# Kernel tuning notes

Measured on AMD Instinct MI355X. Metric: run time of the kernel, lower is better.

## Reference

```python
import jax, jax.numpy as jnp
import numpy as np

HIDDEN = 1024
NUM_HEADS = 16
HEAD_DIM = HIDDEN // NUM_HEADS


def setup_inputs() -> dict:
    key = jax.random.key(0)
    ks = jax.random.split(key, 11)
    s = 1.0 / np.sqrt(HIDDEN)
    x = jax.random.normal(ks[0], (4, 2048, HIDDEN), dtype=jnp.float32)
    Wq = jax.random.uniform(ks[1], (HIDDEN, HIDDEN), jnp.float32, -s, s)
    bq = jax.random.uniform(ks[2], (HIDDEN,), jnp.float32, -s, s)
    Wk = jax.random.uniform(ks[3], (HIDDEN, HIDDEN), jnp.float32, -s, s)
    bk = jax.random.uniform(ks[4], (HIDDEN,), jnp.float32, -s, s)
    Wv = jax.random.uniform(ks[5], (HIDDEN, HIDDEN), jnp.float32, -s, s)
    bv = jax.random.uniform(ks[6], (HIDDEN,), jnp.float32, -s, s)
    Wo = jax.random.uniform(ks[7], (HIDDEN, HIDDEN), jnp.float32, -s, s)
    bo = jax.random.uniform(ks[8], (HIDDEN,), jnp.float32, -s, s)
    ln_g = jnp.ones((HIDDEN,), jnp.float32)
    ln_b = jnp.zeros((HIDDEN,), jnp.float32)
    return {"x": x, "Wq": Wq, "bq": bq, "Wk": Wk, "bk": bk,
            "Wv": Wv, "bv": bv, "Wo": Wo, "bo": bo,
            "ln_g": ln_g, "ln_b": ln_b}


def _layer_norm(x, g, b, eps=1e-5):
    mu = jnp.mean(x, axis=-1, keepdims=True)
    var = jnp.var(x, axis=-1, keepdims=True)
    return (x - mu) * jax.lax.rsqrt(var + eps) * g + b


def reference(x, Wq, bq, Wk, bk, Wv, bv, Wo, bo, ln_g, ln_b):
    B, S, _ = x.shape
    residual = x
    h = _layer_norm(x, ln_g, ln_b)
    # projections (torch Linear: y = h @ W.T + b)
    q = (h @ Wq.T + bq).reshape(B, S, NUM_HEADS, HEAD_DIM).transpose(0, 2, 1, 3)
    k = (h @ Wk.T + bk).reshape(B, S, NUM_HEADS, HEAD_DIM).transpose(0, 2, 1, 3)
    v = (h @ Wv.T + bv).reshape(B, S, NUM_HEADS, HEAD_DIM).transpose(0, 2, 1, 3)
    scores = jnp.einsum('bhqd,bhkd->bhqk', q, k) / np.sqrt(HEAD_DIM).astype(np.float32)
    weights = jax.nn.softmax(scores, axis=-1)  # dropout = identity (eval mode)
    context = jnp.einsum('bhqk,bhkd->bhqd', weights, v)
    context = context.transpose(0, 2, 1, 3).reshape(B, S, HIDDEN)
    out = context @ Wo.T + bo
    return out + residual
```

## Files before the change

### kernel.cpp

```cpp
#include <hip/hip_runtime.h>

typedef unsigned short u16;
typedef unsigned int   u32;
using bf16x8 = __attribute__((ext_vector_type(8))) __bf16;
using f32x4  = __attribute__((ext_vector_type(4))) float;
using u32x2  = __attribute__((ext_vector_type(2))) unsigned int;

__device__ __forceinline__ u16 f2b(float f){
  union { float f; u32 i; } v; v.f = f;
  u32 r = v.i + 0x7FFFu + ((v.i >> 16) & 1u);
  return (u16)(r >> 16);
}
__device__ __forceinline__ u32 pk_bf16_trunc(float a, float b){
  return __builtin_amdgcn_perm(__float_as_uint(b), __float_as_uint(a), 0x07060302u);
}

__global__ __launch_bounds__(256) void cvt_w(const float* __restrict__ s0, const float* __restrict__ s1,
                                             const float* __restrict__ s2, const float* __restrict__ s3,
                                             u16* __restrict__ d){
  const float* srcs[4] = {s0, s1, s2, s3};
  const float* s = srcs[blockIdx.y];
  u16* dd = d + (size_t)blockIdx.y * (1024u * 1024u);
  const int i = (blockIdx.x * 256 + threadIdx.x) * 4;
  float4 v = *(const float4*)(s + i);
  uint2 o;
  o.x = (u32)f2b(v.x) | ((u32)f2b(v.y) << 16);
  o.y = (u32)f2b(v.z) | ((u32)f2b(v.w) << 16);
  *(uint2*)(dd + i) = o;
}

__global__ __launch_bounds__(256) void ln_kernel(const float* __restrict__ x, const float* __restrict__ g,
                                                 const float* __restrict__ be, u16* __restrict__ h){
  const int row = blockIdx.x, tid = threadIdx.x;
  const float* xr = x + (size_t)row * 1024u;
  float4 raw = *(const float4*)(xr + tid * 4);
  float s  = raw.x + raw.y + raw.z + raw.w;
  float sq = raw.x*raw.x + raw.y*raw.y + raw.z*raw.z + raw.w*raw.w;
  #pragma unroll
  for (int m = 1; m < 64; m <<= 1){ s += __shfl_xor(s, m); sq += __shfl_xor(sq, m); }
  __shared__ float ws[4], wq[4];
  if ((tid & 63) == 0){ ws[tid >> 6] = s; wq[tid >> 6] = sq; }
  __syncthreads();
  s  = ws[0] + ws[1] + ws[2] + ws[3];
  sq = wq[0] + wq[1] + wq[2] + wq[3];
  const float mu = s * (1.0f / 1024.0f);
  const float rstd = rsqrtf(sq * (1.0f / 1024.0f) - mu * mu + 1e-5f);
  float4 gg = *(const float4*)(g + tid * 4);
  float4 bb = *(const float4*)(be + tid * 4);
  float y0 = (raw.x - mu) * rstd * gg.x + bb.x;
  float y1 = (raw.y - mu) * rstd * gg.y + bb.y;
  float y2 = (raw.z - mu) * rstd * gg.z + bb.z;
  float y3 = (raw.w - mu) * rstd * gg.w + bb.w;
  uint2 outv;
  outv.x = (u32)f2b(y0) | ((u32)f2b(y1) << 16);
  outv.y = (u32)f2b(y2) | ((u32)f2b(y3) << 16);
  *(uint2*)(h + (size_t)row * 1024u + tid * 4) = outv;
}

__global__ __launch_bounds__(256) void gemm_qkv(const u16* __restrict__ A, const u16* __restrict__ Wcat,
                                                const float* __restrict__ bq, const float* __restrict__ bk,
                                                const float* __restrict__ bv,
                                                u16* __restrict__ qo, u16* __restrict__ ko, u16* __restrict__ vt){
  __shared__ u16 lds[8192];
  u16* lA = lds;
  u16* lB = lds + 4096;
  const int tid = threadIdx.x;
  const int lane = tid & 63, wv = tid >> 6, l15 = lane & 15, quad = lane >> 4;
  const int wr = wv >> 1, wc = wv & 1;
  const int row0 = blockIdx.x * 128, col0 = blockIdx.y * 128;
  const int K = 1024;

  const int r0_ = tid >> 2,         c0_ = tid & 3;
  const int r1_ = (256 + tid) >> 2, c1_ = (256 + tid) & 3;
  const u16* Asrc0 = A    + (size_t)(row0 + r0_) * K + (c0_ ^ ((r0_ >> 1) & 3)) * 8;
  const u16* Asrc1 = A    + (size_t)(row0 + r1_) * K + (c1_ ^ ((r1_ >> 1) & 3)) * 8;
  const u16* Bsrc0 = Wcat + (size_t)(col0 + r0_) * K + (c0_ ^ ((r0_ >> 1) & 3)) * 8;
  const u16* Bsrc1 = Wcat + (size_t)(col0 + r1_) * K + (c1_ ^ ((r1_ >> 1) & 3)) * 8;
  const int cr = (quad ^ ((l15 >> 1) & 3)) * 8;

  f32x4 acc[4][4] = {};
  for (int kt = 0; kt < 32; ++kt){
    __syncthreads();
    __builtin_amdgcn_global_load_lds(
      (const __attribute__((address_space(1))) void*)(Asrc0 + kt * 32),
      (__attribute__((address_space(3))) void*)(&lA[tid * 8]), 16, 0, 0);
    __builtin_amdgcn_global_load_lds(
      (const __attribute__((address_space(1))) void*)(Asrc1 + kt * 32),
      (__attribute__((address_space(3))) void*)(&lA[(256 + tid) * 8]), 16, 0, 0);
    __builtin_amdgcn_global_load_lds(
      (const __attribute__((address_space(1))) void*)(Bsrc0 + kt * 32),
      (__attribute__((address_space(3))) void*)(&lB[tid * 8]), 16, 0, 0);
    __builtin_amdgcn_global_load_lds(
      (const __attribute__((address_space(1))) void*)(Bsrc1 + kt * 32),
      (__attribute__((address_space(3))) void*)(&lB[(256 + tid) * 8]), 16, 0, 0);
    __syncthreads();
    bf16x8 af[4], bf[4];
    #pragma unroll
    for (int i = 0; i < 4; ++i) af[i] = *(const bf16x8*)&lA[(wr * 64 + i * 16 + l15) * 32 + cr];
    #pragma unroll
    for (int j = 0; j < 4; ++j) bf[j] = *(const bf16x8*)&lB[(wc * 64 + j * 16 + l15) * 32 + cr];
    #pragma unroll
    for (int i = 0; i < 4; ++i)
      #pragma unroll
      for (int j = 0; j < 4; ++j)
        acc[i][j] = __builtin_amdgcn_mfma_f32_16x16x32_bf16(af[i], bf[j], acc[i][j], 0, 0, 0);
  }
  const int sel = col0 >> 10;
  if (sel < 2){
    const float* bias = (sel == 0) ? bq : bk;
    u16* dst = (sel == 0) ? qo : ko;
    #pragma unroll
    for (int i = 0; i < 4; ++i){
      const int grow = row0 + wr * 64 + i * 16 + quad * 4;
      #pragma unroll
      for (int j = 0; j < 4; ++j){
        const int gcol = (col0 & 1023) + wc * 64 + j * 16 + l15;
        const float bb = bias[gcol];
        #pragma unroll
        for (int r = 0; r < 4; ++r){
          size_t off = (size_t)(grow + r) * 1024u + gcol;
          dst[off] = f2b(acc[i][j][r] + bb);
        }
      }
    }
  } else {
    __syncthreads();
    u16* pw = lds + wv * 2048;
    const int bglob = row0 >> 11;
    const int head  = ((col0 & 1023) >> 6) + wc;
    const int srem0 = (row0 & 2047) + wr * 64;
    const size_t vbase = (size_t)((bglob * 16 + head) * 64) * 2048u;
    #pragma unroll
    for (int p = 0; p < 2; ++p){
      #pragma unroll
      for (int i2 = 0; i2 < 2; ++i2){
        const int i = p * 2 + i2;
        #pragma unroll
        for (int j = 0; j < 4; ++j){
          const int d = j * 16 + l15;
          const float bv_ = bv[(col0 & 1023) + wc * 64 + d];
          const int u = (i2 * 4 + quad) ^ (d & 7);
          uint2 pk;
          pk.x = (u32)f2b(acc[i][j][0] + bv_) | ((u32)f2b(acc[i][j][1] + bv_) << 16);
          pk.y = (u32)f2b(acc[i][j][2] + bv_) | ((u32)f2b(acc[i][j][3] + bv_) << 16);
          *(uint2*)&pw[d * 32 + u * 4] = pk;
        }
      }
      const int dl = lane;
      #pragma unroll
      for (int c = 0; c < 4; ++c){
        const int u0 = (2 * c) ^ (dl & 7), u1 = (2 * c + 1) ^ (dl & 7);
        uint2 lo = *(const uint2*)&pw[dl * 32 + u0 * 4];
        uint2 hi = *(const uint2*)&pw[dl * 32 + u1 * 4];
        uint4 o4; o4.x = lo.x; o4.y = lo.y; o4.z = hi.x; o4.w = hi.y;
        *(uint4*)(vt + vbase + (size_t)dl * 2048u + srem0 + p * 32 + c * 8) = o4;
      }
    }
  }
}

__global__ __launch_bounds__(256) void gemm_out(const u16* __restrict__ A, const u16* __restrict__ W,
                                                const float* __restrict__ bias, const float* __restrict__ res,
                                                float* __restrict__ C, int M, int N, int K){
  __shared__ u16 lA[128 * 32];
  __shared__ u16 lB[128 * 32];
  const int tid = threadIdx.x;
  const int lane = tid & 63, wv = tid >> 6, l15 = lane & 15, quad = lane >> 4;
  const int wr = wv >> 1, wc = wv & 1;
  const int row0 = blockIdx.x * 128, col0 = blockIdx.y * 128;

  const int r0_ = tid >> 2,         c0_ = tid & 3;
  const int r1_ = (256 + tid) >> 2, c1_ = (256 + tid) & 3;
  const u16* Asrc0 = A + (size_t)(row0 + r0_) * K + (c0_ ^ ((r0_ >> 1) & 3)) * 8;
  const u16* Asrc1 = A + (size_t)(row0 + r1_) * K + (c1_ ^ ((r1_ >> 1) & 3)) * 8;
  const u16* Bsrc0 = W + (size_t)(col0 + r0_) * K + (c0_ ^ ((r0_ >> 1) & 3)) * 8;
  const u16* Bsrc1 = W + (size_t)(col0 + r1_) * K + (c1_ ^ ((r1_ >> 1) & 3)) * 8;
  const int cr = (quad ^ ((l15 >> 1) & 3)) * 8;

  f32x4 acc[4][4] = {};
  const int nkt = K >> 5;
  for (int kt = 0; kt < nkt; ++kt){
    __syncthreads();
    __builtin_amdgcn_global_load_lds(
      (const __attribute__((address_space(1))) void*)(Asrc0 + kt * 32),
      (__attribute__((address_space(3))) void*)(&lA[tid * 8]), 16, 0, 0);
    __builtin_amdgcn_global_load_lds(
      (const __attribute__((address_space(1))) void*)(Asrc1 + kt * 32),
      (__attribute__((address_space(3))) void*)(&lA[(256 + tid) * 8]), 16, 0, 0);
    __builtin_amdgcn_global_load_lds(
      (const __attribute__((address_space(1))) void*)(Bsrc0 + kt * 32),
      (__attribute__((address_space(3))) void*)(&lB[tid * 8]), 16, 0, 0);
    __builtin_amdgcn_global_load_lds(
      (const __attribute__((address_space(1))) void*)(Bsrc1 + kt * 32),
      (__attribute__((address_space(3))) void*)(&lB[(256 + tid) * 8]), 16, 0, 0);
    __syncthreads();
    bf16x8 af[4], bf[4];
    #pragma unroll
    for (int i = 0; i < 4; ++i) af[i] = *(const bf16x8*)&lA[(wr * 64 + i * 16 + l15) * 32 + cr];
    #pragma unroll
    for (int j = 0; j < 4; ++j) bf[j] = *(const bf16x8*)&lB[(wc * 64 + j * 16 + l15) * 32 + cr];
    #pragma unroll
    for (int i = 0; i < 4; ++i)
      #pragma unroll
      for (int j = 0; j < 4; ++j)
        acc[i][j] = __builtin_amdgcn_mfma_f32_16x16x32_bf16(af[i], bf[j], acc[i][j], 0, 0, 0);
  }
  #pragma unroll
  for (int i = 0; i < 4; ++i){
    const int grow = row0 + wr * 64 + i * 16 + quad * 4;
    #pragma unroll
    for (int j = 0; j < 4; ++j){
      const int gcol = col0 + wc * 64 + j * 16 + l15;
      const float bb = bias[gcol];
      #pragma unroll
      for (int r = 0; r < 4; ++r){
        size_t off = (size_t)(grow + r) * N + gcol;
        C[off] = acc[i][j][r] + bb + res[off];
      }
    }
  }
}

__global__ __launch_bounds__(256, 2) void attn_kernel(const u16* __restrict__ Q, const u16* __restrict__ K,
                                                      const u16* __restrict__ Vt, u16* __restrict__ O){
  __shared__ u16 kls[2][64 * 64];
  __shared__ u16 vls[2][64 * 64];
  const int tid = threadIdx.x;
  const int lane = tid & 63, wv = tid >> 6, l15 = lane & 15, quad = lane >> 4;
  const int bh = blockIdx.x & 63, qt = blockIdx.x >> 6;
  const int b = bh >> 4, hh = bh & 15;
  const int q0 = qt * 256;
  const u16* Qg = Q + ((size_t)b * 2048u) * 1024u + hh * 64;
  const u16* Kg = K + ((size_t)b * 2048u) * 1024u + hh * 64;
  const u16* Vg = Vt + (size_t)bh * 64u * 2048u;
  u16* Og = O + ((size_t)b * 2048u) * 1024u + hh * 64;

  const int sr = tid >> 3, sc = tid & 7, sr2 = sr + 32;
  const int sx = (sc ^ (sr & 7)) * 8;
  const int c0 = ((quad ^ (l15 & 7))) * 8;

  const float QSCALE = 0.125f * 1.44269504f;
  bf16x8 qf2[4][2];
  #pragma unroll
  for (int g = 0; g < 4; ++g)
    #pragma unroll
    for (int kk = 0; kk < 2; ++kk){
      qf2[g][kk] = *(const bf16x8*)(Qg + (size_t)(q0 + wv * 64 + g * 16 + l15) * 1024u + kk * 32 + quad * 8);
      #pragma unroll
      for (int e = 0; e < 8; ++e) qf2[g][kk][e] = (__bf16)((float)qf2[g][kk][e] * QSCALE);
    }

  bf16x8 ones_f;
  {
    const __bf16 onev = (__bf16)1.0f, zerov = (__bf16)0.0f;
    #pragma unroll
    for (int e = 0; e < 8; ++e) ones_f[e] = (l15 == 0) ? onev : zerov;
  }

  f32x4 o2[4][4] = {};
  f32x4 o_l[4] = {};
  const f32x4 zf = {0.f, 0.f, 0.f, 0.f};

  uint4 kr0, kr1, vr0, vr1;
  kr0 = *(const uint4*)(Kg + (size_t)sr  * 1024u + sc * 8);
  vr0 = *(const uint4*)(Vg + (size_t)sr  * 2048u + sc * 8);
  kr1 = *(const uint4*)(Kg + (size_t)sr2 * 1024u + sc * 8);
  vr1 = *(const uint4*)(Vg + (size_t)sr2 * 2048u + sc * 8);
  *(uint4*)&kls[0][sr  * 64 + sx] = kr0;
  *(uint4*)&vls[0][sr  * 64 + sx] = vr0;
  *(uint4*)&kls[0][sr2 * 64 + sx] = kr1;
  *(uint4*)&vls[0][sr2 * 64 + sx] = vr1;
  kr0 = *(const uint4*)(Kg + (size_t)(64 + sr)  * 1024u + sc * 8);
  vr0 = *(const uint4*)(Vg + (size_t)sr  * 2048u + 64 + sc * 8);
  kr1 = *(const uint4*)(Kg + (size_t)(64 + sr2) * 1024u + sc * 8);
  vr1 = *(const uint4*)(Vg + (size_t)sr2 * 2048u + 64 + sc * 8);
  __syncthreads();

  for (int kt = 0; kt < 32; ++kt){
    const int cur = kt & 1;
    const u16* kb = kls[cur];
    const u16* vb = vls[cur];
    if (kt < 31){
      u16* kw = kls[cur ^ 1];
      u16* vw = vls[cur ^ 1];
      *(uint4*)&kw[sr  * 64 + sx] = kr0;
      *(uint4*)&vw[sr  * 64 + sx] = vr0;
      *(uint4*)&kw[sr2 * 64 + sx] = kr1;
      *(uint4*)&vw[sr2 * 64 + sx] = vr1;
    }
    if (kt < 30){
      const int s0 = (kt + 2) * 64;
      kr0 = *(const uint4*)(Kg + (size_t)(s0 + sr)  * 1024u + sc * 8);
      vr0 = *(const uint4*)(Vg + (size_t)sr  * 2048u + s0 + sc * 8);
      kr1 = *(const uint4*)(Kg + (size_t)(s0 + sr2) * 1024u + sc * 8);
      vr1 = *(const uint4*)(Vg + (size_t)sr2 * 2048u + s0 + sc * 8);
    }

    f32x4 s2[4][4];
    #pragma unroll
    for (int j = 0; j < 4; ++j){
      const int rb = (j * 16 + l15) * 64;
      bf16x8 kfr0 = *(const bf16x8*)&kb[rb + c0];
      bf16x8 kfr1 = *(const bf16x8*)&kb[rb + (c0 ^ 32)];
      #pragma unroll
      for (int g = 0; g < 4; ++g){
        f32x4 a = __builtin_amdgcn_mfma_f32_16x16x32_bf16(kfr0, qf2[g][0], zf, 0, 0, 0);
        s2[g][j] = __builtin_amdgcn_mfma_f32_16x16x32_bf16(kfr1, qf2[g][1], a, 0, 0, 0);
      }
    }

    #pragma unroll
    for (int g = 0; g < 4; ++g)
      #pragma unroll
      for (int j = 0; j < 4; ++j)
        #pragma unroll
        for (int r = 0; r < 4; ++r)
          s2[g][j][r] = __builtin_amdgcn_exp2f(s2[g][j][r]);

    #pragma unroll
    for (int kk = 0; kk < 2; ++kk){
      bf16x8 afr[4];
      #pragma unroll
      for (int g = 0; g < 4; ++g){
        const int j0 = kk * 2, j1 = j0 + 1;
        u32 A0 = pk_bf16_trunc(s2[g][j0][0], s2[g][j0][1]);
        u32 A1 = pk_bf16_trunc(s2[g][j0][2], s2[g][j0][3]);
        u32 B0 = pk_bf16_trunc(s2[g][j1][0], s2[g][j1][1]);
        u32 B1 = pk_bf16_trunc(s2[g][j1][2], s2[g][j1][3]);
        u32x2 r1 = __builtin_amdgcn_permlane32_swap(A0, B0, false, false);
        u32x2 r2 = __builtin_amdgcn_permlane16_swap(r1[0], r1[1], false, false);
        u32x2 r3 = __builtin_amdgcn_permlane32_swap(A1, B1, false, false);
        u32x2 r4 = __builtin_amdgcn_permlane16_swap(r3[0], r3[1], false, false);
        union { uint4 u; bf16x8 v; } cv;
        cv.u.x = r2[0]; cv.u.y = r4[0]; cv.u.z = r2[1]; cv.u.w = r4[1];
        afr[g] = cv.v;
      }
      #pragma unroll
      for (int g = 0; g < 4; ++g)
        o_l[g] = __builtin_amdgcn_mfma_f32_16x16x32_bf16(afr[g], ones_f, o_l[g], 0, 0, 0);
      #pragma unroll
      for (int j2 = 0; j2 < 4; ++j2){
        bf16x8 bfr = *(const bf16x8*)&vb[(j2 * 16 + l15) * 64 + (c0 ^ (kk * 32))];
        #pragma unroll
        for (int g = 0; g < 4; ++g)
          o2[g][j2] = __builtin_amdgcn_mfma_f32_16x16x32_bf16(afr[g], bfr, o2[g][j2], 0, 0, 0);
      }
    }
    __syncthreads();
  }

  #pragma unroll
  for (int g = 0; g < 4; ++g){
    float lr[4];
    #pragma unroll
    for (int r = 0; r < 4; ++r) lr[r] = 1.0f / __shfl(o_l[g][r], quad * 16);
    #pragma unroll
    for (int j2 = 0; j2 < 4; ++j2){
      #pragma unroll
      for (int r = 0; r < 4; ++r){
        const int qrow = q0 + wv * 64 + g * 16 + quad * 4 + r;
        const int d = j2 * 16 + l15;
        Og[(size_t)qrow * 1024u + d] = f2b(o2[g][j2][r] * lr[r]);
      }
    }
  }
}

extern "C" void kernel_launch(void* const* d_in, const int* in_sizes, int n_in,
                              void* d_out, int out_size, void* d_ws, size_t ws_size,
                              hipStream_t stream){
  (void)in_sizes; (void)n_in; (void)out_size; (void)ws_size;
  const float* x   = (const float*)d_in[0];
  const float* Wq  = (const float*)d_in[1];
  const float* bq  = (const float*)d_in[2];
  const float* Wk  = (const float*)d_in[3];
  const float* bk  = (const float*)d_in[4];
  const float* Wv  = (const float*)d_in[5];
  const float* bv  = (const float*)d_in[6];
  const float* Wo  = (const float*)d_in[7];
  const float* bo  = (const float*)d_in[8];
  const float* lng = (const float*)d_in[9];
  const float* lnb = (const float*)d_in[10];
  float* out = (float*)d_out;

  const size_t TE = (size_t)8192 * 1024;
  u16* ws0 = (u16*)d_ws;
  u16* ws1 = ws0 + TE;
  u16* ws2 = ws1 + TE;
  u16* wsw = ws2 + TE;
  u16* wob = wsw + (size_t)3 * 1024 * 1024;
  u16* vt  = (u16*)d_out;

  cvt_w<<<dim3(1024, 4), 256, 0, stream>>>(Wq, Wk, Wv, Wo, wsw);
  ln_kernel<<<dim3(8192), 256, 0, stream>>>(x, lng, lnb, ws0);
  gemm_qkv<<<dim3(64, 24), 256, 0, stream>>>(ws0, wsw, bq, bk, bv, ws1, ws2, vt);
  attn_kernel<<<dim3(512), 256, 0, stream>>>(ws1, ws2, vt, ws1);
  gemm_out<<<dim3(64, 8), 256, 0, stream>>>(ws1, wob, bo, x, out, 8192, 1024, 1024);
}
```

Before: 275.4 us.

## Double-buffer LDS with register prefetch in QKV and output GEMMs

```diff
diff --git a/kernel.cpp b/kernel.cpp
--- a/kernel.cpp
+++ b/kernel.cpp
@@ -61,9 +61,8 @@
                                                 const float* __restrict__ bq, const float* __restrict__ bk,
                                                 const float* __restrict__ bv,
                                                 u16* __restrict__ qo, u16* __restrict__ ko, u16* __restrict__ vt){
-  __shared__ u16 lds[8192];
-  u16* lA = lds;
-  u16* lB = lds + 4096;
+  __shared__ u16 lA[2][4096];
+  __shared__ u16 lB[2][4096];
   const int tid = threadIdx.x;
   const int lane = tid & 63, wv = tid >> 6, l15 = lane & 15, quad = lane >> 4;
   const int wr = wv >> 1, wc = wv & 1;
@@ -79,31 +78,47 @@
   const int cr = (quad ^ ((l15 >> 1) & 3)) * 8;
 
   f32x4 acc[4][4] = {};
+  uint4 ar0, ar1, br0, br1;
+  ar0 = *(const uint4*)(Asrc0);
+  ar1 = *(const uint4*)(Asrc1);
+  br0 = *(const uint4*)(Bsrc0);
+  br1 = *(const uint4*)(Bsrc1);
+  *(uint4*)&lA[0][tid * 8] = ar0;
+  *(uint4*)&lA[0][(256 + tid) * 8] = ar1;
+  *(uint4*)&lB[0][tid * 8] = br0;
+  *(uint4*)&lB[0][(256 + tid) * 8] = br1;
+  ar0 = *(const uint4*)(Asrc0 + 32);
+  ar1 = *(const uint4*)(Asrc1 + 32);
+  br0 = *(const uint4*)(Bsrc0 + 32);
+  br1 = *(const uint4*)(Bsrc1 + 32);
+  __syncthreads();
+
   for (int kt = 0; kt < 32; ++kt){
-    __syncthreads();
-    __builtin_amdgcn_global_load_lds(
-      (const __attribute__((address_space(1))) void*)(Asrc0 + kt * 32),
-      (__attribute__((address_space(3))) void*)(&lA[tid * 8]), 16, 0, 0);
-    __builtin_amdgcn_global_load_lds(
-      (const __attribute__((address_space(1))) void*)(Asrc1 + kt * 32),
-      (__attribute__((address_space(3))) void*)(&lA[(256 + tid) * 8]), 16, 0, 0);
-    __builtin_amdgcn_global_load_lds(
-      (const __attribute__((address_space(1))) void*)(Bsrc0 + kt * 32),
-      (__attribute__((address_space(3))) void*)(&lB[tid * 8]), 16, 0, 0);
-    __builtin_amdgcn_global_load_lds(
-      (const __attribute__((address_space(1))) void*)(Bsrc1 + kt * 32),
-      (__attribute__((address_space(3))) void*)(&lB[(256 + tid) * 8]), 16, 0, 0);
-    __syncthreads();
+    const int cur = kt & 1;
+    if (kt < 31){
+      *(uint4*)&lA[cur ^ 1][tid * 8] = ar0;
+      *(uint4*)&lA[cur ^ 1][(256 + tid) * 8] = ar1;
+      *(uint4*)&lB[cur ^ 1][tid * 8] = br0;
+      *(uint4*)&lB[cur ^ 1][(256 + tid) * 8] = br1;
+    }
+    if (kt < 30){
+      const int o = (kt + 2) * 32;
+      ar0 = *(const uint4*)(Asrc0 + o);
+      ar1 = *(const uint4*)(Asrc1 + o);
+      br0 = *(const uint4*)(Bsrc0 + o);
+      br1 = *(const uint4*)(Bsrc1 + o);
+    }
     bf16x8 af[4], bf[4];
     #pragma unroll
-    for (int i = 0; i < 4; ++i) af[i] = *(const bf16x8*)&lA[(wr * 64 + i * 16 + l15) * 32 + cr];
-    #pragma unroll
-    for (int j = 0; j < 4; ++j) bf[j] = *(const bf16x8*)&lB[(wc * 64 + j * 16 + l15) * 32 + cr];
+    for (int i = 0; i < 4; ++i) af[i] = *(const bf16x8*)&lA[cur][(wr * 64 + i * 16 + l15) * 32 + cr];
+    #pragma unroll
+    for (int j = 0; j < 4; ++j) bf[j] = *(const bf16x8*)&lB[cur][(wc * 64 + j * 16 + l15) * 32 + cr];
     #pragma unroll
     for (int i = 0; i < 4; ++i)
       #pragma unroll
       for (int j = 0; j < 4; ++j)
         acc[i][j] = __builtin_amdgcn_mfma_f32_16x16x32_bf16(af[i], bf[j], acc[i][j], 0, 0, 0);
+    __syncthreads();
   }
   const int sel = col0 >> 10;
   if (sel < 2){
@@ -124,8 +139,7 @@
       }
     }
   } else {
-    __syncthreads();
-    u16* pw = lds + wv * 2048;
+    u16* pw = &lA[0][0] + wv * 2048;
     const int bglob = row0 >> 11;
     const int head  = ((col0 & 1023) >> 6) + wc;
     const int srem0 = (row0 & 2047) + wr * 64;
@@ -162,8 +176,8 @@
 __global__ __launch_bounds__(256) void gemm_out(const u16* __restrict__ A, const u16* __restrict__ W,
                                                 const float* __restrict__ bias, const float* __restrict__ res,
                                                 float* __restrict__ C, int M, int N, int K){
-  __shared__ u16 lA[128 * 32];
-  __shared__ u16 lB[128 * 32];
+  __shared__ u16 lA[2][4096];
+  __shared__ u16 lB[2][4096];
   const int tid = threadIdx.x;
   const int lane = tid & 63, wv = tid >> 6, l15 = lane & 15, quad = lane >> 4;
   const int wr = wv >> 1, wc = wv & 1;
@@ -179,31 +193,47 @@
 
   f32x4 acc[4][4] = {};
   const int nkt = K >> 5;
+  uint4 ar0, ar1, br0, br1;
+  ar0 = *(const uint4*)(Asrc0);
+  ar1 = *(const uint4*)(Asrc1);
+  br0 = *(const uint4*)(Bsrc0);
+  br1 = *(const uint4*)(Bsrc1);
+  *(uint4*)&lA[0][tid * 8] = ar0;
+  *(uint4*)&lA[0][(256 + tid) * 8] = ar1;
+  *(uint4*)&lB[0][tid * 8] = br0;
+  *(uint4*)&lB[0][(256 + tid) * 8] = br1;
+  ar0 = *(const uint4*)(Asrc0 + 32);
+  ar1 = *(const uint4*)(Asrc1 + 32);
+  br0 = *(const uint4*)(Bsrc0 + 32);
+  br1 = *(const uint4*)(Bsrc1 + 32);
+  __syncthreads();
+
   for (int kt = 0; kt < nkt; ++kt){
-    __syncthreads();
-    __builtin_amdgcn_global_load_lds(
-      (const __attribute__((address_space(1))) void*)(Asrc0 + kt * 32),
-      (__attribute__((address_space(3))) void*)(&lA[tid * 8]), 16, 0, 0);
-    __builtin_amdgcn_global_load_lds(
-      (const __attribute__((address_space(1))) void*)(Asrc1 + kt * 32),
-      (__attribute__((address_space(3))) void*)(&lA[(256 + tid) * 8]), 16, 0, 0);
-    __builtin_amdgcn_global_load_lds(
-      (const __attribute__((address_space(1))) void*)(Bsrc0 + kt * 32),
-      (__attribute__((address_space(3))) void*)(&lB[tid * 8]), 16, 0, 0);
-    __builtin_amdgcn_global_load_lds(
-      (const __attribute__((address_space(1))) void*)(Bsrc1 + kt * 32),
-      (__attribute__((address_space(3))) void*)(&lB[(256 + tid) * 8]), 16, 0, 0);
-    __syncthreads();
+    const int cur = kt & 1;
+    if (kt < nkt - 1){
+      *(uint4*)&lA[cur ^ 1][tid * 8] = ar0;
+      *(uint4*)&lA[cur ^ 1][(256 + tid) * 8] = ar1;
+      *(uint4*)&lB[cur ^ 1][tid * 8] = br0;
+      *(uint4*)&lB[cur ^ 1][(256 + tid) * 8] = br1;
+    }
+    if (kt < nkt - 2){
+      const int o = (kt + 2) * 32;
+      ar0 = *(const uint4*)(Asrc0 + o);
+      ar1 = *(const uint4*)(Asrc1 + o);
+      br0 = *(const uint4*)(Bsrc0 + o);
+      br1 = *(const uint4*)(Bsrc1 + o);
+    }
     bf16x8 af[4], bf[4];
     #pragma unroll
-    for (int i = 0; i < 4; ++i) af[i] = *(const bf16x8*)&lA[(wr * 64 + i * 16 + l15) * 32 + cr];
-    #pragma unroll
-    for (int j = 0; j < 4; ++j) bf[j] = *(const bf16x8*)&lB[(wc * 64 + j * 16 + l15) * 32 + cr];
+    for (int i = 0; i < 4; ++i) af[i] = *(const bf16x8*)&lA[cur][(wr * 64 + i * 16 + l15) * 32 + cr];
+    #pragma unroll
+    for (int j = 0; j < 4; ++j) bf[j] = *(const bf16x8*)&lB[cur][(wc * 64 + j * 16 + l15) * 32 + cr];
     #pragma unroll
     for (int i = 0; i < 4; ++i)
       #pragma unroll
       for (int j = 0; j < 4; ++j)
         acc[i][j] = __builtin_amdgcn_mfma_f32_16x16x32_bf16(af[i], bf[j], acc[i][j], 0, 0, 0);
+    __syncthreads();
   }
   #pragma unroll
   for (int i = 0; i < 4; ++i){
```

Measured after the change: 267.0 us. -3.0%, faster.
